# Optimization experiments

Hardware: AMD Instinct MI355X
Metric: run time of the kernel (lower is better)

Reference implementation:

```python
import jax, jax.numpy as jnp
import numpy as np
import math

# Model dims (match init_kwargs)
H = 4096      # hidden_size
NH = 32       # num attention heads
NKV = 8       # num kv heads
D = 128       # head_dim
S = 2048      # num tokens
WINDOW = 1024 # sliding window (layer_idx=0 -> active)
SCALE = D ** -0.5
# YaRN rope params from GptOssConfig.rope_parameters
BASE = 500000.0
FACTOR = 4.0
ORIG_MAX = 32768
BETA_FAST = 32
BETA_SLOW = 1


def _yarn_cos_sin(positions):
    """YaRN-scaled rotary cos/sin, NEOX style. Returns ([S, D/2], [S, D/2])."""
    d2 = D // 2
    pos_freqs = BASE ** (np.arange(d2, dtype=np.float64) * 2.0 / D)
    inv_extra = 1.0 / pos_freqs
    inv_inter = 1.0 / (FACTOR * pos_freqs)

    def corr_dim(n):
        return (D * math.log(ORIG_MAX / (n * 2 * math.pi))) / (2 * math.log(BASE))

    low = max(math.floor(corr_dim(BETA_FAST)), 0)
    high = min(math.ceil(corr_dim(BETA_SLOW)), d2 - 1)
    ramp = np.clip((np.arange(d2, dtype=np.float64) - low) / max(high - low, 0.001), 0.0, 1.0)
    mask = 1.0 - ramp  # 1 -> extrapolation (high freq), 0 -> interpolation (low freq)
    inv_freq = inv_inter * (1.0 - mask) + inv_extra * mask
    mscale = 0.1 * math.log(FACTOR) + 1.0
    freqs = positions.astype(jnp.float32)[:, None] * jnp.asarray(inv_freq, dtype=jnp.float32)[None, :]
    return jnp.cos(freqs) * mscale, jnp.sin(freqs) * mscale


def _rope(x, cos, sin):
    # x: [S, h, D]; rotate-halves (NEOX)
    x1, x2 = jnp.split(x, 2, axis=-1)
    c, s = cos[:, None, :], sin[:, None, :]
    return jnp.concatenate([x1 * c - x2 * s, x2 * c + x1 * s], axis=-1)


def reference(hidden_states, positions, qkv_w, qkv_b, o_w, o_b, sinks):
    qs, kvs = NH * D, NKV * D
    qkv = hidden_states @ qkv_w.T + qkv_b                  # [S, qs + 2*kvs]
    q = qkv[:, :qs].reshape(S, NH, D)
    k = qkv[:, qs:qs + kvs].reshape(S, NKV, D)
    v = qkv[:, qs + kvs:].reshape(S, NKV, D)

    cos, sin = _yarn_cos_sin(positions)
    q = _rope(q, cos, sin)
    k = _rope(k, cos, sin)

    # GQA: expand kv heads to match q heads
    g = NH // NKV
    k = jnp.repeat(k, g, axis=1)                            # [S, NH, D]
    v = jnp.repeat(v, g, axis=1)

    scores = jnp.einsum('qhd,khd->hqk', q, k) * SCALE       # [NH, S, S]
    i = jnp.arange(S)[:, None]
    j = jnp.arange(S)[None, :]
    allowed = (j <= i) & ((i - j) < WINDOW)                 # causal + sliding window
    scores = jnp.where(allowed[None, :, :], scores, -jnp.inf)

    # sink-aware softmax: learned per-head sink logit joins the normalization
    m = jnp.maximum(jnp.max(scores, axis=-1), sinks[:, None])   # [NH, S]
    e = jnp.exp(scores - m[..., None])                          # masked -> exp(-inf)=0
    denom = e.sum(-1) + jnp.exp(sinks[:, None] - m)             # [NH, S]
    probs = e / denom[..., None]

    attn = jnp.einsum('hqk,khd->qhd', probs, v).reshape(S, NH * D)
    return attn @ o_w.T + o_b


def setup_inputs() -> dict:
    key = jax.random.key(0)
    k1, k2, k3, k4, k5 = jax.random.split(key, 5)
    w_scale = 0.02
    return {
        'hidden_states': jax.random.normal(k1, (S, H), dtype=jnp.float32),
        'positions': jnp.arange(S, dtype=jnp.int64) if jax.config.jax_enable_x64 else jnp.arange(S, dtype=jnp.int32),
        'qkv_w': jax.random.normal(k2, (NH * D + 2 * NKV * D, H), dtype=jnp.float32) * w_scale,
        'qkv_b': jax.random.normal(k3, (NH * D + 2 * NKV * D,), dtype=jnp.float32) * w_scale,
        'o_w': jax.random.normal(k4, (H, H), dtype=jnp.float32) * w_scale,
        'o_b': jax.random.normal(k5, (H,), dtype=jnp.float32) * w_scale,
        'sinks': jnp.zeros((NH,), dtype=jnp.float32),
    }
```

## Files before the change

### kernel.cpp

```cpp
#include <hip/hip_runtime.h>

#define S_LEN   2048
#define HID     4096
#define NH      32
#define NKV     8
#define HD      128
#define QKV_N   (NH*HD + 2*NKV*HD)
#define WINDOW  1024

typedef unsigned short u16;
typedef short s8v  __attribute__((ext_vector_type(8)));
typedef short s4v  __attribute__((ext_vector_type(4)));
typedef float f4v  __attribute__((ext_vector_type(4)));

#define MFMA16x32(a, b, c) __builtin_amdgcn_mfma_f32_16x16x32_bf16(a, b, c, 0, 0, 0)

typedef __attribute__((address_space(1))) const unsigned int g_u32;
typedef __attribute__((address_space(3))) unsigned int l_u32;

__device__ __forceinline__ float bf2f(u16 h) {
  union { unsigned int u; float f; } x;
  x.u = ((unsigned int)h) << 16;
  return x.f;
}
__device__ __forceinline__ u16 f2bf(float f) {
  union { float f; unsigned int u; } x;
  x.f = f;
  unsigned int u = x.u;
  return (u16)((u + 0x7FFFu + ((u >> 16) & 1u)) >> 16);
}

__global__ __launch_bounds__(256) void cvt_bf16(const float* __restrict__ in,
                                               u16* __restrict__ out) {
  int i = (blockIdx.x * 256 + threadIdx.x) * 4;
  float4 v = *(const float4*)&in[i];
  u16 h[4] = { f2bf(v.x), f2bf(v.y), f2bf(v.z), f2bf(v.w) };
  *(s4v*)&out[i] = *(const s4v*)h;
}

template<int OUT_BF16>
__global__ __launch_bounds__(256) void gemm_bt(
    const u16* __restrict__ A, const u16* __restrict__ B,
    const float* __restrict__ bias, void* __restrict__ Cp,
    int M, int N, int K)
{
  __shared__ __align__(16) u16 sA[128 * 32];
  __shared__ __align__(16) u16 sB[128 * 32];
  const int tid  = threadIdx.x;
  const int lane = tid & 63;
  const int w    = tid >> 6;
  const int wr   = w >> 1, wc = w & 1;
  const int ln   = lane & 15, quad = lane >> 4;
  const long mBase = (long)blockIdx.y * 128;
  const long nBase = (long)blockIdx.x * 128;

  f4v acc[4][4];
#pragma unroll
  for (int i = 0; i < 4; ++i)
#pragma unroll
    for (int j = 0; j < 4; ++j)
#pragma unroll
      for (int r = 0; r < 4; ++r) acc[i][j][r] = 0.0f;

  const int steps = K >> 5;
  for (int kt = 0; kt < steps; ++kt) {
    __syncthreads();
#pragma unroll
    for (int p = 0; p < 2; ++p) {
      int c = p * 256 + tid;
      int row = c >> 2, col = (c & 3) << 3;
      const u16* ga = A + (mBase + row) * (long)K + kt * 32 + col;
      const u16* gb = B + (nBase + row) * (long)K + kt * 32 + col;
      u16* la = sA + (p * 256 + w * 64) * 8;
      u16* lb = sB + (p * 256 + w * 64) * 8;
      __builtin_amdgcn_global_load_lds((g_u32*)(const void*)ga, (l_u32*)(void*)la, 16, 0, 0);
      __builtin_amdgcn_global_load_lds((g_u32*)(const void*)gb, (l_u32*)(void*)lb, 16, 0, 0);
    }
    __syncthreads();

    s8v af[4], bfr[4];
#pragma unroll
    for (int i = 0; i < 4; ++i)
      af[i] = *(const s8v*)&sA[(wr * 64 + i * 16 + ln) * 32 + quad * 8];
#pragma unroll
    for (int j = 0; j < 4; ++j)
      bfr[j] = *(const s8v*)&sB[(wc * 64 + j * 16 + ln) * 32 + quad * 8];
#pragma unroll
    for (int i = 0; i < 4; ++i)
#pragma unroll
      for (int j = 0; j < 4; ++j)
        acc[i][j] = MFMA16x32(af[i], bfr[j], acc[i][j]);
  }

#pragma unroll
  for (int i = 0; i < 4; ++i) {
    long rowb = mBase + wr * 64 + i * 16 + quad * 4;
#pragma unroll
    for (int j = 0; j < 4; ++j) {
      long col = nBase + wc * 64 + j * 16 + ln;
      float bv = bias[col];
#pragma unroll
      for (int r = 0; r < 4; ++r) {
        float v = acc[i][j][r] + bv;
        if (OUT_BF16) ((u16*)Cp)[(rowb + r) * (long)N + col] = f2bf(v);
        else          ((float*)Cp)[(rowb + r) * (long)N + col] = v;
      }
    }
  }
}

__global__ __launch_bounds__(256) void rope_split(
    const u16* __restrict__ qkv, const int* __restrict__ positions,
    u16* __restrict__ qo, u16* __restrict__ ko, u16* __restrict__ vo)
{
  const int s = blockIdx.x;
  const int t = threadIdx.x;
  __shared__ float csh[64], snh[64];

  if (t < 64) {
    const double LN_BASE = log(500000.0);
    const double TWO_PI  = 6.283185307179586476925287;
    double cf  = 128.0 * log(32768.0 / (32.0 * TWO_PI)) / (2.0 * LN_BASE);
    double cs_ = 128.0 * log(32768.0 / TWO_PI) / (2.0 * LN_BASE);
    double lowd  = floor(cf);  if (lowd < 0.0)  lowd = 0.0;
    double highd = ceil(cs_);  if (highd > 63.0) highd = 63.0;
    double denom = highd - lowd; if (denom < 0.001) denom = 0.001;
    double d = (double)t;
    double inv_extra = exp(-LN_BASE * d / 64.0);
    double inv_inter = inv_extra * 0.25;
    double ramp = (d - lowd) / denom;
    ramp = ramp < 0.0 ? 0.0 : (ramp > 1.0 ? 1.0 : ramp);
    double maskv = 1.0 - ramp;
    double invf = inv_inter * (1.0 - maskv) + inv_extra * maskv;
    float freq = (float)positions[s] * (float)invf;
    const float msc = 1.1386294361119891f;
    csh[t] = cosf(freq) * msc;
    snh[t] = sinf(freq) * msc;
  }
  __syncthreads();

  const u16* row = qkv + (size_t)s * QKV_N;
  const float SC = 0.08838834764831845f;

#pragma unroll
  for (int i = 0; i < 8; ++i) {
    int p = i * 256 + t;
    int hh = p >> 6, d = p & 63;
    float x1 = bf2f(row[hh * 128 + d]), x2 = bf2f(row[hh * 128 + d + 64]);
    float c = csh[d], sn = snh[d];
    qo[(size_t)s * 4096 + hh * 128 + d]      = f2bf((x1 * c - x2 * sn) * SC);
    qo[(size_t)s * 4096 + hh * 128 + d + 64] = f2bf((x2 * c + x1 * sn) * SC);
  }
#pragma unroll
  for (int i = 0; i < 2; ++i) {
    int p = i * 256 + t;
    int hh = p >> 6, d = p & 63;
    float x1 = bf2f(row[4096 + hh * 128 + d]), x2 = bf2f(row[4096 + hh * 128 + d + 64]);
    float c = csh[d], sn = snh[d];
    ko[(size_t)s * 1024 + hh * 128 + d]      = f2bf(x1 * c - x2 * sn);
    ko[(size_t)s * 1024 + hh * 128 + d + 64] = f2bf(x2 * c + x1 * sn);
  }
#pragma unroll
  for (int i = 0; i < 4; ++i) {
    int e = i * 256 + t;
    vo[(size_t)s * 1024 + e] = row[5120 + e];
  }
}

__global__ __launch_bounds__(256) void transpose_v(const u16* __restrict__ vb,
                                                   u16* __restrict__ vt) {
  __shared__ u16 tile[64][72];
  const int s0 = blockIdx.x * 64, c0 = blockIdx.y * 64;
  const int tid = threadIdx.x;
#pragma unroll
  for (int t = 0; t < 2; ++t) {
    int row = t * 32 + (tid >> 3), col = (tid & 7) * 8;
    *(s8v*)&tile[row][col] = *(const s8v*)&vb[(size_t)(s0 + row) * 1024 + c0 + col];
  }
  __syncthreads();
#pragma unroll
  for (int t = 0; t < 2; ++t) {
    int orow = t * 32 + (tid >> 3), ocol = (tid & 7) * 8;
    u16 v[8];
#pragma unroll
    for (int e = 0; e < 8; ++e) v[e] = tile[ocol + e][orow];
    *(s8v*)&vt[(size_t)(c0 + orow) * 2048 + s0 + ocol] = *(const s8v*)v;
  }
}

__global__ __launch_bounds__(256) void attn_fwd(
    const u16* __restrict__ Q, const u16* __restrict__ Kb,
    const u16* __restrict__ Vt, const float* __restrict__ sinks,
    u16* __restrict__ O)
{
  const int h = blockIdx.y, kvh = h >> 2;
  const int q0 = blockIdx.x * 64;
  const int tid = threadIdx.x, w = tid >> 6, lane = tid & 63;
  const int ln = lane & 15, quad = lane >> 4;
  const int qw = q0 + w * 16;
  const int qi = qw + ln;

  __shared__ __align__(16) u16 sK[64 * 136];
  __shared__ __align__(16) u16 sVt[128 * 72];
  __shared__ __align__(16) u16 sP[4][16 * 72];

  s8v qf[4];
  {
    const u16* qrow = Q + (size_t)qi * 4096 + h * 128;
#pragma unroll
    for (int kb = 0; kb < 4; ++kb)
      qf[kb] = *(const s8v*)&qrow[kb * 32 + quad * 8];
  }

  float m_v = sinks[h], l_v = 1.0f;
  f4v accO[8];
#pragma unroll
  for (int j = 0; j < 8; ++j)
#pragma unroll
    for (int r = 0; r < 4; ++r) accO[j][r] = 0.0f;

  int lo = q0 - (WINDOW - 1); if (lo < 0) lo = 0; lo &= ~63;

  for (int kt = lo; kt <= q0; kt += 64) {
    __syncthreads();
#pragma unroll
    for (int t = 0; t < 4; ++t) {
      int c = t * 256 + tid;
      int row = c >> 4, col = (c & 15) * 8;
      *(s8v*)&sK[row * 136 + col] =
          *(const s8v*)&Kb[(size_t)(kt + row) * 1024 + kvh * 128 + col];
    }
#pragma unroll
    for (int t = 0; t < 4; ++t) {
      int c = t * 256 + tid;
      int row = c >> 3, col = (c & 7) * 8;
      *(s8v*)&sVt[row * 72 + col] =
          *(const s8v*)&Vt[(size_t)(kvh * 128 + row) * 2048 + kt + col];
    }
    __syncthreads();

    f4v sc[4];
    bool dead[4];
#pragma unroll
    for (int h4 = 0; h4 < 4; ++h4) {
      const int kb16 = kt + h4 * 16;
      dead[h4] = (kb16 > qw + 15) || (kb16 + 15 < qw - (WINDOW - 1));
      if (dead[h4]) {
#pragma unroll
        for (int r = 0; r < 4; ++r) sc[h4][r] = -1e30f;
        continue;
      }
      f4v s;
#pragma unroll
      for (int r = 0; r < 4; ++r) s[r] = 0.0f;
#pragma unroll
      for (int kb = 0; kb < 4; ++kb) {
        s8v kf = *(const s8v*)&sK[(h4 * 16 + ln) * 136 + kb * 32 + quad * 8];
        s = MFMA16x32(kf, qf[kb], s);
      }
      const bool full = (kb16 + 15 <= qw) && (qw + 15 - kb16 <= WINDOW - 1);
      if (!full) {
        int base = qi - kb16 - quad * 4;
#pragma unroll
        for (int r = 0; r < 4; ++r)
          s[r] = ((unsigned)(base - r) <= (WINDOW - 1)) ? s[r] : -1e30f;
      }
      sc[h4] = s;
    }

    float mn = m_v;
#pragma unroll
    for (int h4 = 0; h4 < 4; ++h4)
#pragma unroll
      for (int r = 0; r < 4; ++r) mn = fmaxf(mn, sc[h4][r]);
    mn = fmaxf(mn, __shfl_xor(mn, 16));
    mn = fmaxf(mn, __shfl_xor(mn, 32));

    float alpha = __expf(m_v - mn);
    m_v = mn;
    l_v *= alpha;
#pragma unroll
    for (int j = 0; j < 8; ++j)
#pragma unroll
      for (int r = 0; r < 4; ++r) accO[j][r] *= alpha;

    float lsum = 0.0f;
#pragma unroll
    for (int h4 = 0; h4 < 4; ++h4) {
      float p[4];
#pragma unroll
      for (int r = 0; r < 4; ++r) p[r] = __expf(sc[h4][r] - mn);
      lsum += (p[0] + p[1]) + (p[2] + p[3]);
      u16 pb[4] = { f2bf(p[0]), f2bf(p[1]), f2bf(p[2]), f2bf(p[3]) };
      *(s4v*)&sP[w][ln * 72 + h4 * 16 + quad * 4] = *(const s4v*)pb;
    }
    lsum += __shfl_xor(lsum, 16);
    lsum += __shfl_xor(lsum, 32);
    l_v += lsum;

    __syncthreads();

#pragma unroll
    for (int c2 = 0; c2 < 2; ++c2) {
      if (dead[2 * c2] && dead[2 * c2 + 1]) continue;
      s8v pf = *(const s8v*)&sP[w][ln * 72 + c2 * 32 + quad * 8];
#pragma unroll
      for (int j = 0; j < 8; ++j) {
        s8v vf = *(const s8v*)&sVt[(j * 16 + ln) * 72 + c2 * 32 + quad * 8];
        accO[j] = MFMA16x32(vf, pf, accO[j]);
      }
    }
  }

  __syncthreads();
  u16* sO = sK;
  const float rl = 1.0f / l_v;
#pragma unroll
  for (int j = 0; j < 8; ++j) {
    u16 ob[4] = { f2bf(accO[j][0] * rl), f2bf(accO[j][1] * rl),
                  f2bf(accO[j][2] * rl), f2bf(accO[j][3] * rl) };
    *(s4v*)&sO[(w * 16 + ln) * 136 + j * 16 + quad * 4] = *(const s4v*)ob;
  }
  __syncthreads();
  {
    int row = lane >> 2, cc = lane & 3;
#pragma unroll
    for (int i = 0; i < 4; ++i) {
      s8v v = *(const s8v*)&sO[(w * 16 + row) * 136 + cc * 8 + i * 32];
      *(s8v*)&O[(size_t)(q0 + w * 16 + row) * 4096 + h * 128 + cc * 8 + i * 32] = v;
    }
  }
}

extern "C" void kernel_launch(void* const* d_in, const int* in_sizes, int n_in,
                              void* d_out, int out_size, void* d_ws, size_t ws_size,
                              hipStream_t stream) {
  const float* hidden    = (const float*)d_in[0];
  const int*   positions = (const int*)d_in[1];
  const float* qkv_w     = (const float*)d_in[2];
  const float* qkv_b     = (const float*)d_in[3];
  const float* o_w       = (const float*)d_in[4];
  const float* o_b       = (const float*)d_in[5];
  const float* sinks     = (const float*)d_in[6];

  char* ws = (char*)d_ws;
  u16* wW   = (u16*)ws;
  u16* qb   = (u16*)ws;
  u16* kb   = (u16*)(ws + 16777216ull);
  u16* vb   = (u16*)(ws + 20971520ull);
  u16* vt   = (u16*)(ws + 25165824ull);
  u16* attn = (u16*)(ws + 29360128ull);
  u16* hb   = (u16*)(ws + 50331648ull);
  u16* qkvb = (u16*)(ws + 67108864ull);
  u16* oWb  = (u16*)(ws + 50331648ull);

  cvt_bf16<<<8192, 256, 0, stream>>>(hidden, hb);
  cvt_bf16<<<24576, 256, 0, stream>>>(qkv_w, wW);

  gemm_bt<1><<<dim3(QKV_N / 128, S_LEN / 128), 256, 0, stream>>>(
      hb, wW, qkv_b, (void*)qkvb, S_LEN, QKV_N, HID);

  rope_split<<<S_LEN, 256, 0, stream>>>(qkvb, positions, qb, kb, vb);

  cvt_bf16<<<16384, 256, 0, stream>>>(o_w, oWb);

  transpose_v<<<dim3(32, 16), 256, 0, stream>>>(vb, vt);

  attn_fwd<<<dim3(S_LEN / 64, NH), 256, 0, stream>>>(qb, kb, vt, sinks, attn);

  gemm_bt<0><<<dim3(HID / 128, S_LEN / 128), 256, 0, stream>>>(
      attn, oWb, o_b, d_out, S_LEN, HID, HID);
}
```

Before: 556.7 us.

## Load K/V MFMA fragments directly from global memory, drop shared staging and block barriers

The attention kernel no longer stages K and V^T tiles into shared memory. Each wave reads its MFMA fragments straight from global memory (relying on L2/cache reuse across the four waves and GQA heads), and the block-wide __syncthreads are replaced with per-wave lgkmcnt waits since sP and sO are now private to each wave. s_setprio is raised around MFMA bursts. This removes LDS traffic and barrier stalls, but the kernel now issues redundant global loads, with each wave fetching the same K/V rows, and depends on the cache to absorb them.

```diff
diff --git a/kernel.cpp b/kernel.cpp
--- a/kernel.cpp
+++ b/kernel.cpp
@@ -200,9 +200,8 @@
   const int qw = q0 + w * 16;
   const int qi = qw + ln;
 
-  __shared__ __align__(16) u16 sK[64 * 136];
-  __shared__ __align__(16) u16 sVt[128 * 72];
   __shared__ __align__(16) u16 sP[4][16 * 72];
+  __shared__ __align__(16) u16 sO[64 * 136];
 
   s8v qf[4];
   {
@@ -221,24 +220,10 @@
 
   int lo = q0 - (WINDOW - 1); if (lo < 0) lo = 0; lo &= ~63;
 
+  const u16* Kh = Kb + (size_t)kvh * 128 + quad * 8;
+  const u16* Vh = Vt + ((size_t)kvh * 128 + ln) * 2048 + quad * 8;
+
   for (int kt = lo; kt <= q0; kt += 64) {
-    __syncthreads();
-#pragma unroll
-    for (int t = 0; t < 4; ++t) {
-      int c = t * 256 + tid;
-      int row = c >> 4, col = (c & 15) * 8;
-      *(s8v*)&sK[row * 136 + col] =
-          *(const s8v*)&Kb[(size_t)(kt + row) * 1024 + kvh * 128 + col];
-    }
-#pragma unroll
-    for (int t = 0; t < 4; ++t) {
-      int c = t * 256 + tid;
-      int row = c >> 3, col = (c & 7) * 8;
-      *(s8v*)&sVt[row * 72 + col] =
-          *(const s8v*)&Vt[(size_t)(kvh * 128 + row) * 2048 + kt + col];
-    }
-    __syncthreads();
-
     f4v sc[4];
     bool dead[4];
 #pragma unroll
@@ -250,14 +235,20 @@
         for (int r = 0; r < 4; ++r) sc[h4][r] = -1e30f;
         continue;
       }
+      const u16* krow = Kh + (size_t)(kb16 + ln) * 1024;
+      s8v kf0 = *(const s8v*)&krow[0];
+      s8v kf1 = *(const s8v*)&krow[32];
+      s8v kf2 = *(const s8v*)&krow[64];
+      s8v kf3 = *(const s8v*)&krow[96];
       f4v s;
 #pragma unroll
       for (int r = 0; r < 4; ++r) s[r] = 0.0f;
-#pragma unroll
-      for (int kb = 0; kb < 4; ++kb) {
-        s8v kf = *(const s8v*)&sK[(h4 * 16 + ln) * 136 + kb * 32 + quad * 8];
-        s = MFMA16x32(kf, qf[kb], s);
-      }
+      __builtin_amdgcn_s_setprio(1);
+      s = MFMA16x32(kf0, qf[0], s);
+      s = MFMA16x32(kf1, qf[1], s);
+      s = MFMA16x32(kf2, qf[2], s);
+      s = MFMA16x32(kf3, qf[3], s);
+      __builtin_amdgcn_s_setprio(0);
       const bool full = (kb16 + 15 <= qw) && (qw + 15 - kb16 <= WINDOW - 1);
       if (!full) {
         int base = qi - kb16 - quad * 4;
@@ -298,22 +289,24 @@
     lsum += __shfl_xor(lsum, 32);
     l_v += lsum;
 
-    __syncthreads();
+    asm volatile("s_waitcnt lgkmcnt(0)" ::: "memory");
+    __builtin_amdgcn_sched_barrier(0);
 
 #pragma unroll
     for (int c2 = 0; c2 < 2; ++c2) {
       if (dead[2 * c2] && dead[2 * c2 + 1]) continue;
       s8v pf = *(const s8v*)&sP[w][ln * 72 + c2 * 32 + quad * 8];
+      const u16* vrow = Vh + kt + c2 * 32;
+      __builtin_amdgcn_s_setprio(1);
 #pragma unroll
       for (int j = 0; j < 8; ++j) {
-        s8v vf = *(const s8v*)&sVt[(j * 16 + ln) * 72 + c2 * 32 + quad * 8];
+        s8v vf = *(const s8v*)&vrow[(size_t)j * 16 * 2048];
         accO[j] = MFMA16x32(vf, pf, accO[j]);
       }
-    }
-  }
-
-  __syncthreads();
-  u16* sO = sK;
+      __builtin_amdgcn_s_setprio(0);
+    }
+  }
+
   const float rl = 1.0f / l_v;
 #pragma unroll
   for (int j = 0; j < 8; ++j) {
@@ -321,7 +314,8 @@
                   f2bf(accO[j][2] * rl), f2bf(accO[j][3] * rl) };
     *(s4v*)&sO[(w * 16 + ln) * 136 + j * 16 + quad * 4] = *(const s4v*)ob;
   }
-  __syncthreads();
+  asm volatile("s_waitcnt lgkmcnt(0)" ::: "memory");
+  __builtin_amdgcn_sched_barrier(0);
   {
     int row = lane >> 2, cc = lane & 3;
 #pragma unroll
```

After: 747.6 us. 1.34x slower.

## Rewrite GEMM with 128x256 tiles, triple-buffered async LDS pipeline and swizzle

Applied to the files above, without the earlier changes.

Replaces the single-buffered 128x128, K=32 GEMM with a 512-thread, 128x256-tile kernel using K=64 tiles. Global-to-LDS loads run two tiles ahead across three LDS buffers, with XOR swizzling to avoid bank conflicts and setprio around the MFMA bursts. The aim is to overlap memory latency with MFMA work and raise data reuse for both GEMMs. In exchange it uses 144KB of LDS per block, which limits occupancy, and the hand-placed waitcnt and barrier logic is easy to get wrong.

```diff
diff --git a/kernel.cpp b/kernel.cpp
--- a/kernel.cpp
+++ b/kernel.cpp
@@ -39,20 +39,22 @@
 }
 
 template<int OUT_BF16>
-__global__ __launch_bounds__(256) void gemm_bt(
+__global__ __launch_bounds__(512, 2) void gemm_bt(
     const u16* __restrict__ A, const u16* __restrict__ B,
     const float* __restrict__ bias, void* __restrict__ Cp,
     int M, int N, int K)
 {
-  __shared__ __align__(16) u16 sA[128 * 32];
-  __shared__ __align__(16) u16 sB[128 * 32];
+  __shared__ __align__(16) char lds[3 * 49152];
   const int tid  = threadIdx.x;
   const int lane = tid & 63;
   const int w    = tid >> 6;
-  const int wr   = w >> 1, wc = w & 1;
+  const int wm   = w >> 2, wn = w & 3;
   const int ln   = lane & 15, quad = lane >> 4;
   const long mBase = (long)blockIdx.y * 128;
-  const long nBase = (long)blockIdx.x * 128;
+  const long nBase = (long)blockIdx.x * 256;
+  const u16* Ab = A + mBase * (long)K;
+  const u16* Bb = B + nBase * (long)K;
+  const long rs = (long)K * 2;
 
   f4v acc[4][4];
 #pragma unroll
@@ -62,42 +64,87 @@
 #pragma unroll
       for (int r = 0; r < 4; ++r) acc[i][j][r] = 0.0f;
 
-  const int steps = K >> 5;
-  for (int kt = 0; kt < steps; ++kt) {
-    __syncthreads();
-#pragma unroll
-    for (int p = 0; p < 2; ++p) {
-      int c = p * 256 + tid;
-      int row = c >> 2, col = (c & 3) << 3;
-      const u16* ga = A + (mBase + row) * (long)K + kt * 32 + col;
-      const u16* gb = B + (nBase + row) * (long)K + kt * 32 + col;
-      u16* la = sA + (p * 256 + w * 64) * 8;
-      u16* lb = sB + (p * 256 + w * 64) * 8;
-      __builtin_amdgcn_global_load_lds((g_u32*)(const void*)ga, (l_u32*)(void*)la, 16, 0, 0);
-      __builtin_amdgcn_global_load_lds((g_u32*)(const void*)gb, (l_u32*)(void*)lb, 16, 0, 0);
-    }
-    __syncthreads();
-
-    s8v af[4], bfr[4];
-#pragma unroll
-    for (int i = 0; i < 4; ++i)
-      af[i] = *(const s8v*)&sA[(wr * 64 + i * 16 + ln) * 32 + quad * 8];
-#pragma unroll
-    for (int j = 0; j < 4; ++j)
-      bfr[j] = *(const s8v*)&sB[(wc * 64 + j * 16 + ln) * 32 + quad * 8];
-#pragma unroll
-    for (int i = 0; i < 4; ++i)
-#pragma unroll
-      for (int j = 0; j < 4; ++j)
-        acc[i][j] = MFMA16x32(af[i], bfr[j], acc[i][j]);
+  const int nt = K >> 6;
+
+  auto stage = [&](int tile, int i0, int i1) {
+    char* base = lds + (tile % 3) * 49152;
+    const int ktb = tile * 128;
+#pragma unroll
+    for (int k = i0; k < i1; ++k) {
+      const u16* gsrc = (k < 2) ? Ab : Bb;
+      char* ldst      = (k < 2) ? base : (base + 16384);
+      const int kk    = (k < 2) ? k : (k - 2);
+      int o  = kk * 8192 + w * 1024 + lane * 16;
+      int o2 = o ^ ((o >> 4) & 0x60);
+      const char* gp = (const char*)gsrc + (long)(o2 >> 7) * rs + ktb + (o2 & 127);
+      __builtin_amdgcn_global_load_lds((g_u32*)(const void*)gp,
+                                       (l_u32*)(void*)(ldst + kk * 8192 + w * 1024),
+                                       16, 0, 0);
+    }
+  };
+
+  stage(0, 0, 6);
+  stage(1, 0, 6);
+  asm volatile("s_waitcnt vmcnt(6)" ::: "memory");
+  __builtin_amdgcn_sched_barrier(0);
+  __builtin_amdgcn_s_barrier();
+
+  int bsel = 0;
+  for (int t = 0; t < nt; ++t) {
+    char* base = lds + bsel * 49152;
+    const bool doStage = (t + 2 < nt);
+
+#pragma unroll
+    for (int ks = 0; ks < 2; ++ks) {
+      s8v af[4], bf[4];
+#pragma unroll
+      for (int f = 0; f < 4; ++f) {
+        int r = wm * 64 + f * 16 + ln;
+        int o = r * 128 + ks * 64 + quad * 16;
+        o ^= (r & 12) << 3;
+        af[f] = *(const s8v*)(base + o);
+      }
+#pragma unroll
+      for (int j = 0; j < 4; ++j) {
+        int r = wn * 64 + j * 16 + ln;
+        int o = r * 128 + ks * 64 + quad * 16;
+        o ^= (r & 12) << 3;
+        bf[j] = *(const s8v*)(base + 16384 + o);
+      }
+      if (doStage) {
+        if (ks == 0) stage(t + 2, 0, 3);
+        else         stage(t + 2, 3, 6);
+      }
+      __builtin_amdgcn_s_barrier();
+      asm volatile("s_waitcnt lgkmcnt(0)" ::: "memory");
+      __builtin_amdgcn_sched_barrier(0);
+      __builtin_amdgcn_s_setprio(1);
+#pragma unroll
+      for (int i = 0; i < 4; ++i)
+#pragma unroll
+        for (int j = 0; j < 4; ++j)
+          acc[i][j] = MFMA16x32(af[i], bf[j], acc[i][j]);
+      __builtin_amdgcn_s_setprio(0);
+    }
+
+    if (t < nt - 2) {
+      asm volatile("s_waitcnt vmcnt(6)" ::: "memory");
+      __builtin_amdgcn_sched_barrier(0);
+      __builtin_amdgcn_s_barrier();
+    } else if (t == nt - 2) {
+      asm volatile("s_waitcnt vmcnt(0)" ::: "memory");
+      __builtin_amdgcn_sched_barrier(0);
+      __builtin_amdgcn_s_barrier();
+    }
+    bsel = (bsel == 2) ? 0 : bsel + 1;
   }
 
 #pragma unroll
   for (int i = 0; i < 4; ++i) {
-    long rowb = mBase + wr * 64 + i * 16 + quad * 4;
+    long rowb = mBase + wm * 64 + i * 16 + quad * 4;
 #pragma unroll
     for (int j = 0; j < 4; ++j) {
-      long col = nBase + wc * 64 + j * 16 + ln;
+      long col = nBase + wn * 64 + j * 16 + ln;
       float bv = bias[col];
 #pragma unroll
       for (int r = 0; r < 4; ++r) {
@@ -357,7 +404,7 @@
   cvt_bf16<<<8192, 256, 0, stream>>>(hidden, hb);
   cvt_bf16<<<24576, 256, 0, stream>>>(qkv_w, wW);
 
-  gemm_bt<1><<<dim3(QKV_N / 128, S_LEN / 128), 256, 0, stream>>>(
+  gemm_bt<1><<<dim3(QKV_N / 256, S_LEN / 128), 512, 0, stream>>>(
       hb, wW, qkv_b, (void*)qkvb, S_LEN, QKV_N, HID);
 
   rope_split<<<S_LEN, 256, 0, stream>>>(qkvb, positions, qb, kb, vb);
@@ -368,6 +415,6 @@
 
   attn_fwd<<<dim3(S_LEN / 64, NH), 256, 0, stream>>>(qb, kb, vt, sinks, attn);
 
-  gemm_bt<0><<<dim3(HID / 128, S_LEN / 128), 256, 0, stream>>>(
+  gemm_bt<0><<<dim3(HID / 256, S_LEN / 128), 512, 0, stream>>>(
       attn, oWb, o_b, d_out, S_LEN, HID, HID);
 }
```

After: 525.2 us. 1.06x faster.
